# Kernel tuning notes

Measured on AMD Instinct MI355X. Metric: run time of the kernel, lower is better.

The kernel has to match this reference:

```python
import jax, jax.numpy as jnp
import numpy as np

EPS = 1e-5

def _ternary_ste(w):
    # STEQuantize: round(w/scale) clamped to [-1,1]; straight-through gradient.
    scale = jnp.maximum(jnp.mean(jnp.abs(w)), EPS)
    q = jnp.clip(jnp.round(w / scale), -1.0, 1.0)
    return w + jax.lax.stop_gradient(q - w)

def _bitlinear(x, w):
    # BitLinear: y = x @ (ternary(w) * scale)^T, scale = mean|w| (differentiable).
    scale = jnp.maximum(jnp.mean(jnp.abs(w)), EPS)
    return x @ (_ternary_ste(w) * scale).T

def _op_library(x, indices, weights, ops):
    # ops: (n_ops, D, D). Per-op ternary quantize + scale, then one batched einsum
    # instead of the python loop of small matmuls.
    n_ops = ops.shape[0]
    scales = jnp.maximum(jnp.mean(jnp.abs(ops), axis=(1, 2)), EPS)  # (n_ops,)
    q = jnp.clip(jnp.round(ops / scales[:, None, None]), -1.0, 1.0)
    w_eff = (ops + jax.lax.stop_gradient(q - ops)) * scales[:, None, None]  # (n,o,d)
    # transformed[n] = x @ w_eff[n]^T  ->  (B, S, n_ops, D)
    T = jnp.einsum('bsd,nod->bsno', x, w_eff)
    out = (1e-5 / n_ops) * jnp.sum(T, axis=2)
    gathered = jnp.take_along_axis(T, indices[:, :, :, None], axis=2)  # (B,S,K,D)
    out = out + jnp.sum(weights[..., None] * gathered, axis=2)
    return out

def _mem_read(x, slots, W_read):
    d = slots.shape[1]
    key = x @ W_read.T
    attn = jax.nn.softmax(key @ slots.T / jnp.sqrt(jnp.float32(d)), axis=-1)
    return attn @ slots

def _layernorm(x, gamma, beta):
    mu = jnp.mean(x, axis=-1, keepdims=True)
    var = jnp.var(x, axis=-1, keepdims=True)
    return (x - mu) * jax.lax.rsqrt(var + EPS) * gamma + beta

def _single_pass(reason, ops, W_router, slots, W_read, W_mix, ln_gamma, ln_beta, top_k):
    logits = _bitlinear(reason, W_router)              # (B,S,n_ops)
    vals, indices = jax.lax.top_k(logits, top_k)       # (B,S,K)
    weights = jax.nn.softmax(vals, axis=-1)
    op_out = _op_library(reason, indices, weights, ops)
    mem_out = _mem_read(reason, slots, W_read)
    mixed = jnp.concatenate([op_out, mem_out], axis=-1) @ W_mix.T
    return _layernorm(reason + mixed, ln_gamma, ln_beta)

def _write_signal(q, slots, W_wk, W_wg, W_wv):
    d = slots.shape[1]
    wk = q @ W_wk.T
    wg = jax.nn.sigmoid(q @ W_wg.T)                    # (B,S,1)
    wv = q @ W_wv.T
    addr = jax.nn.softmax(wk @ slots.T / jnp.sqrt(jnp.float32(d)), axis=-1)
    return wg * wv + 0.1 * (addr @ slots)

def setup_inputs() -> dict:
    key = jax.random.key(0)
    ks = jax.random.split(key, 12)
    B, S, d_model, d_reason = 8, 2048, 1024, 128
    n_ops, n_slots = 32, 16
    return {
        'hidden': jax.random.normal(ks[0], (B, S, d_model), jnp.float32),
        'force_depth': 2,
        'W_down': jax.random.normal(ks[1], (d_reason, d_model), jnp.float32) * 0.02,
        'W_up': jax.random.normal(ks[2], (d_model, d_reason), jnp.float32) * 0.02,
        'ops': jax.random.normal(ks[3], (n_ops, d_reason, d_reason), jnp.float32) * 0.02,
        'W_router': jax.random.normal(ks[4], (n_ops, d_reason), jnp.float32) * 0.02,
        'slots': jax.random.normal(ks[5], (n_slots, d_reason), jnp.float32) * 0.01,
        'W_read': jax.random.normal(ks[6], (d_reason, d_reason), jnp.float32) * 0.02,
        'W_wk': jax.random.normal(ks[7], (d_reason, d_reason), jnp.float32) * 0.02,
        'W_wg': jax.random.normal(ks[8], (1, d_reason), jnp.float32) * 0.02,
        'W_wv': jax.random.normal(ks[9], (d_reason, d_reason), jnp.float32) * 0.02,
        'W_mix': jax.random.normal(ks[10], (d_reason, 2 * d_reason), jnp.float32) * 0.02,
        'ln_gamma': jnp.ones((d_reason,), jnp.float32),
        'ln_beta': jnp.zeros((d_reason,), jnp.float32),
        'write_scale': jnp.float32(0.01),
    }

def reference(hidden, force_depth, W_down, W_up, ops, W_router, slots, W_read,
              W_wk, W_wg, W_wv, W_mix, ln_gamma, ln_beta, write_scale):
    top_k = 2
    reason = _bitlinear(hidden, W_down)
    for _ in range(int(force_depth)):
        reason = _single_pass(reason, ops, W_router, slots, W_read, W_mix,
                              ln_gamma, ln_beta, top_k)
    reason = reason + write_scale * _write_signal(reason, slots, W_wk, W_wg, W_wv)
    out = _bitlinear(reason, W_up)
    return hidden + out
```

## Files before the change

### kernel.cpp

```cpp
#include <hip/hip_runtime.h>


#define DR   128
#define DM   1024
#define NTOK 16384
#define NOPS 32
#define COEF (1e-5f / 32.f)

typedef __attribute__((ext_vector_type(8))) short bfrag;
typedef __attribute__((ext_vector_type(4))) float f32x4;

__device__ __forceinline__ ushort f2b_bits(float f) {
  union { float f; uint i; } c; c.f = f;
  uint x = c.i;
  return (ushort)((x + 0x7fffu + ((x >> 16) & 1u)) >> 16);
}
__device__ __forceinline__ float qeff(float w, float s) {
  float q = rintf(w / s);
  q = fminf(1.f, fmaxf(-1.f, q));
  return q * s;
}
__device__ __forceinline__ float waveRed(float v) {
#pragma unroll
  for (int m = 32; m > 0; m >>= 1) v += __shfl_xor(v, m, 64);
// ... 11 lines not shown
#define OFF_MRS     (OFF_WWVB + 32768)
#define OFF_MWS     (OFF_MRS + 8192)
#define OFF_SB      (OFF_MWS + 8192)
#define OFF_SLOTS   (OFF_SB + 8192)
#define OFF_WWG     (OFF_SLOTS + 8192)
#define OFF_GAMMA   (OFF_WWG + 512)
#define OFF_BETA    (OFF_GAMMA + 512)
#define OFF_WSC     (OFF_BETA + 512)
#define OFF_RF      (OFF_WSC + 256)
#define WS_TOTAL    (OFF_RF + 4194304)

__global__ __launch_bounds__(256) void k_absum_all(
    const float* __restrict__ W_down, const float* __restrict__ W_router,
    const float* __restrict__ W_up, const float* __restrict__ ops,
    float* __restrict__ sums) {
  __shared__ float ws4[4];
  const int y = blockIdx.y;
  const float* src; int n; float* dst;
  if (y == 0)      { src = W_down;   n = 131072; dst = &sums[0]; }
  else if (y == 1) { src = W_router; n = 4096;   dst = &sums[1]; }
  else if (y == 2) { src = W_up;     n = 131072; dst = &sums[2]; }
  else { src = ops + (size_t)(y - 3) * 16384; n = 16384; dst = &sums[y]; }
  float s = 0.f;
  for (int i = blockIdx.x * 256 + threadIdx.x; i < n; i += 8 * 256)
    s += fabsf(src[i]);
  s = waveRed(s);
  int lane = threadIdx.x & 63, wv = threadIdx.x >> 6;
  if (lane == 0) ws4[wv] = s;
  __syncthreads();
  if (threadIdx.x == 0) atomicAdd(dst, ws4[0] + ws4[1] + ws4[2] + ws4[3]);
}

__global__ __launch_bounds__(256) void k_build(
    const float* __restrict__ W_down, const float* __restrict__ W_up,
    const float* __restrict__ W_router, const float* __restrict__ ops,
    const float* __restrict__ W_read, const float* __restrict__ W_wk,
    const float* __restrict__ W_wg, const float* __restrict__ W_wv,
    const float* __restrict__ W_mix, const float* __restrict__ slots,
    const float* __restrict__ gamma, const float* __restrict__ beta,
    const float* __restrict__ wscale, int has_wsc, const float* __restrict__ sums,
    ushort* __restrict__ WdE, ushort* __restrict__ WuE, float* __restrict__ WrT,
    ushort* __restrict__ opsB, float* __restrict__ opsScale,
    ushort* __restrict__ WmixA, ushort* __restrict__ WwvB,
    float* __restrict__ Mrs, float* __restrict__ Mws, float* __restrict__ SBw,
    float* __restrict__ slotsF, float* __restrict__ WwgF,
    float* __restrict__ gammaF, float* __restrict__ betaF, float* __restrict__ wscF) {
  int id = blockIdx.x * 256 + threadIdx.x;
  const float s_wd = fmaxf(sums[0] * (1.f / 131072.f), 1e-5f);
  const float s_wr = fmaxf(sums[1] * (1.f / 4096.f), 1e-5f);
  const float s_wu = fmaxf(sums[2] * (1.f / 131072.f), 1e-5f);

  if (id < 131072) { WdE[id] = f2b_bits(qeff(W_down[id], s_wd)); return; }
  id -= 131072;
  if (id < 131072) { WuE[id] = f2b_bits(qeff(W_up[id], s_wu)); return; }
  id -= 131072;
  if (id < 4096) {
    int d = id >> 5, n = id & 31;
    WrT[id] = qeff(W_router[n * DR + d], s_wr);
    return;
  }
  id -= 4096;
  if (id < 524288) {
    int n = id >> 14;
    float s = fmaxf(sums[3 + n] * (1.f / 16384.f), 1e-5f);
    float q = rintf(ops[id] / s);
    q = fminf(1.f, fmaxf(-1.f, q));
    opsB[id] = f2b_bits(q);
    return;
  }
  id -= 524288;
  if (id < 32) { opsScale[id] = fmaxf(sums[3 + id] * (1.f / 16384.f), 1e-5f); return; }
  id -= 32;
  if (id < 16384) {
    int r = id >> 7, o = id & 127;
    WmixA[id] = f2b_bits(W_mix[r * 256 + o]);
    return;
  }
  id -= 16384;
  if (id < 16384) { WwvB[id] = f2b_bits(W_wv[id]); return; }
  id -= 16384;
  if (id < 2048) {
    int d = id >> 4, j = id & 15;
    float a = 0.f;
    for (int o = 0; o < DR; ++o) a += W_read[o * DR + d] * slots[j * DR + o];
    Mrs[id] = a;
    return;
  }
  id -= 2048;
  if (id < 2048) {
    int d = id >> 4, j = id & 15;
    float a = 0.f;
    for (int o = 0; o < DR; ++o) a += W_wk[o * DR + d] * slots[j * DR + o];
    Mws[id] = a;
    return;
  }
  id -= 2048;
  if (id < 2048) {
    int j = id >> 7, r = id & 127;
    float a = 0.f;
    for (int o = 0; o < DR; ++o) a += slots[j * DR + o] * W_mix[r * 256 + 128 + o];
    SBw[id] = a;
    return;
  }
  id -= 2048;
  if (id < 2048) { slotsF[id] = slots[id]; return; }
  id -= 2048;
  if (id < 128) { WwgF[id] = W_wg[id]; return; }
  id -= 128;
  if (id < 128) { gammaF[id] = gamma[id]; return; }
  id -= 128;
  if (id < 128) { betaF[id] = beta[id]; return; }
  id -= 128;
  if (id == 0) { wscF[0] = has_wsc ? wscale[0] : 0.01f; }
}

__global__ __launch_bounds__(256) void k_down(const float* __restrict__ hidden,
                                              const ushort* __restrict__ WdE,
                                              float* __restrict__ X) {
  const int w = threadIdx.x >> 6, lane = threadIdx.x & 63;
  const int quad = lane >> 4, mrow = lane & 15;
  const int m0 = blockIdx.x * 16;
  const int c0 = w * 32;

  f32x4 acc[2];
  acc[0] = (f32x4){0.f, 0.f, 0.f, 0.f};
  acc[1] = (f32x4){0.f, 0.f, 0.f, 0.f};

  const float* Ap = hidden + (size_t)(m0 + mrow) * DM + quad * 8;
#pragma unroll 2
  for (int kt = 0; kt < 32; ++kt) {
    float4 a0 = *(const float4*)(Ap + kt * 32);
    float4 a1 = *(const float4*)(Ap + kt * 32 + 4);
    bfrag a;
    a[0] = (short)f2b_bits(a0.x); a[1] = (short)f2b_bits(a0.y);
    a[2] = (short)f2b_bits(a0.z); a[3] = (short)f2b_bits(a0.w);
    a[4] = (short)f2b_bits(a1.x); a[5] = (short)f2b_bits(a1.y);
    a[6] = (short)f2b_bits(a1.z); a[7] = (short)f2b_bits(a1.w);
#pragma unroll
    for (int nt = 0; nt < 2; ++nt) {
      bfrag b = *(const bfrag*)(WdE + (size_t)(c0 + nt * 16 + mrow) * DM + kt * 32 + quad * 8);
      acc[nt] = __builtin_amdgcn_mfma_f32_16x16x32_bf16(a, b, acc[nt], 0, 0, 0);
    }
  }
#pragma unroll
  for (int nt = 0; nt < 2; ++nt)
#pragma unroll
    for (int r = 0; r < 4; ++r)
      X[(size_t)(m0 + quad * 4 + r) * DR + c0 + nt * 16 + mrow] = acc[nt][r];
}

__global__ __launch_bounds__(512) void k_pass2(
    float* __restrict__ X, ushort* __restrict__ RF, int emit,
    const float* __restrict__ WrT, const ushort* __restrict__ opsB,
    const float* __restrict__ opsScale, const ushort* __restrict__ WmixA,
    const float* __restrict__ Mrs, const float* __restrict__ SBw,
    const float* __restrict__ gammaF, const float* __restrict__ betaF,
    const ushort* __restrict__ WwvB, const float* __restrict__ Mws,
    const float* __restrict__ slotsF, const float* __restrict__ WwgF,
    const float* __restrict__ wscF) {
  __shared__ float  xsf[64][128];
  __shared__ ushort xsb[64][136];
  __shared__ float  lg[64][33];
  __shared__ float  coefT[32][64];
  __shared__ float  attn[64][17];
  __shared__ float  at2[64][17];
  __shared__ int    seli[64][2];
  __shared__ float  selw[64][2];
  __shared__ float  gp[64];
  __shared__ float  partS[8][4][4];
  __shared__ float  partQ[8][4][4];

  const int tid = threadIdx.x;
  const int w = tid >> 6, lane = tid & 63;
  const int quad = lane >> 4, mrow = lane & 15;
  const int t0 = blockIdx.x * 64;

  for (int i = tid; i < 2048; i += 512) {
    float4 v = *(const float4*)(X + (size_t)t0 * DR + i * 4);
    int t = i >> 5, c = (i & 31) * 4;
    xsf[t][c] = v.x; xsf[t][c + 1] = v.y; xsf[t][c + 2] = v.z; xsf[t][c + 3] = v.w;
    xsb[t][c] = f2b_bits(v.x); xsb[t][c + 1] = f2b_bits(v.y);
    xsb[t][c + 2] = f2b_bits(v.z); xsb[t][c + 3] = f2b_bits(v.w);
  }
  __syncthreads();

  for (int p = tid; p < 2048; p += 512) {
    int t = p >> 5, n = p & 31;
    float a = 0.f;
#pragma unroll 8
    for (int d = 0; d < DR; ++d) a += xsf[t][d] * WrT[d * 32 + n];
    lg[t][n] = a;
  }
  for (int p = tid; p < 1024; p += 512) {
    int t = p >> 4, j = p & 15;
    float a = 0.f;
#pragma unroll 8
    for (int d = 0; d < DR; ++d) a += xsf[t][d] * Mrs[d * 16 + j];
    attn[t][j] = a * 0.088388347648318447f;
  }
  __syncthreads();

  if (tid < 64) {
    float v0 = -1e30f; int i0 = 0;
#pragma unroll
    for (int n = 0; n < 32; ++n) { float v = lg[tid][n]; if (v > v0) { v0 = v; i0 = n; } }
    float v1 = -1e30f; int i1 = 0;
#pragma unroll
    for (int n = 0; n < 32; ++n)
      if (n != i0) { float v = lg[tid][n]; if (v > v1) { v1 = v; i1 = n; } }
    float e = expf(v1 - v0);
    float w0 = 1.f / (1.f + e);
    seli[tid][0] = i0; seli[tid][1] = i1;
    selw[tid][0] = w0; selw[tid][1] = e * w0;
    float m = -1e30f;
#pragma unroll
    for (int j = 0; j < 16; ++j) m = fmaxf(m, attn[tid][j]);
    float s = 0.f;
#pragma unroll
    for (int j = 0; j < 16; ++j) { float ee = expf(attn[tid][j] - m); attn[tid][j] = ee; s += ee; }
    float inv = 1.f / s;
#pragma unroll
    for (int j = 0; j < 16; ++j) attn[tid][j] *= inv;
  }
  __syncthreads();

  for (int p = tid; p < 2048; p += 512) {
    int n = p >> 6, t = p & 63;
    float cf = COEF;
    if (n == seli[t][0]) cf += selw[t][0];
    if (n == seli[t][1]) cf += selw[t][1];
    coefT[n][t] = cf * opsScale[n];
  }
  __syncthreads();

  bfrag a[4][4];
#pragma unroll
  for (int m = 0; m < 4; ++m)
#pragma unroll
    for (int kt = 0; kt < 4; ++kt)
      a[m][kt] = *(const bfrag*)&xsb[m * 16 + mrow][kt * 32 + quad * 8];

  const ushort* Bp = opsB + (size_t)(w * 16 + mrow) * DR + quad * 8;
  bfrag bc[4], bn[4];
#pragma unroll
  for (int kt = 0; kt < 4; ++kt) bc[kt] = *(const bfrag*)(Bp + kt * 32);

  f32x4 out[4];
#pragma unroll
  for (int m = 0; m < 4; ++m) out[m] = (f32x4){0.f, 0.f, 0.f, 0.f};

  for (int n = 0; n < NOPS; ++n) {
    if (n + 1 < NOPS) {
      const ushort* Bn = Bp + (size_t)(n + 1) * (DR * DR);
#pragma unroll
      for (int kt = 0; kt < 4; ++kt) bn[kt] = *(const bfrag*)(Bn + kt * 32);
    }
    f32x4 tmp[4];
#pragma unroll
    for (int m = 0; m < 4; ++m) tmp[m] = (f32x4){0.f, 0.f, 0.f, 0.f};
#pragma unroll
    for (int kt = 0; kt < 4; ++kt)
#pragma unroll
      for (int m = 0; m < 4; ++m)
        tmp[m] = __builtin_amdgcn_mfma_f32_16x16x32_bf16(a[m][kt], bc[kt], tmp[m], 0, 0, 0);
#pragma unroll
    for (int m = 0; m < 4; ++m) {
      f32x4 cf = *(const f32x4*)&coefT[n][m * 16 + quad * 4];
      out[m] += cf * tmp[m];
    }
    if (n + 1 < NOPS) {
#pragma unroll
      for (int kt = 0; kt < 4; ++kt) bc[kt] = bn[kt];
    }
  }
  __syncthreads();

#pragma unroll
  for (int m = 0; m < 4; ++m)
#pragma unroll
    for (int r = 0; r < 4; ++r)
      xsb[m * 16 + quad * 4 + r][w * 16 + mrow] = f2b_bits(out[m][r]);
  __syncthreads();

  const int mtile = w & 3;
  const int ch = (w >> 2) * 64;
  {
    bfrag a2[4];
#pragma unroll
    for (int kt = 0; kt < 4; ++kt)
      a2[kt] = *(const bfrag*)&xsb[mtile * 16 + mrow][kt * 32 + quad * 8];

    f32x4 acc[4];
#pragma unroll
    for (int i = 0; i < 4; ++i) acc[i] = (f32x4){0.f, 0.f, 0.f, 0.f};
#pragma unroll
    for (int kt = 0; kt < 4; ++kt)
#pragma unroll
      for (int nt = 0; nt < 4; ++nt) {
        bfrag b = *(const bfrag*)(WmixA + (size_t)(ch + nt * 16 + mrow) * DR + kt * 32 + quad * 8);
        acc[nt] = __builtin_amdgcn_mfma_f32_16x16x32_bf16(a2[kt], b, acc[nt], 0, 0, 0);
      }

    float v[4][4];
#pragma unroll
    for (int nt = 0; nt < 4; ++nt) {
      const int col = ch + nt * 16 + mrow;
#pragma unroll
      for (int r = 0; r < 4; ++r) {
        const int t = mtile * 16 + quad * 4 + r;
        float y0 = 0.f;
#pragma unroll
        for (int j = 0; j < 16; ++j) y0 += attn[t][j] * SBw[j * 128 + col];
        v[nt][r] = acc[nt][r] + xsf[t][col] + y0;
      }
    }
    float s[4], q[4];
#pragma unroll
    for (int r = 0; r < 4; ++r) {
      float ps = 0.f, pq = 0.f;
#pragma unroll
      for (int nt = 0; nt < 4; ++nt) { ps += v[nt][r]; pq += v[nt][r] * v[nt][r]; }
      s[r] = ps; q[r] = pq;
    }
#pragma unroll
    for (int m = 1; m < 16; m <<= 1)
#pragma unroll
      for (int r = 0; r < 4; ++r) {
        s[r] += __shfl_xor(s[r], m, 64);
        q[r] += __shfl_xor(q[r], m, 64);
      }
    if (mrow == 0)
#pragma unroll
      for (int r = 0; r < 4; ++r) { partS[w][quad][r] = s[r]; partQ[w][quad][r] = q[r]; }
    __syncthreads();

    float mu[4], rsd[4];
#pragma unroll
    for (int r = 0; r < 4; ++r) {
      float ts = s[r] + partS[w ^ 4][quad][r];
      float tq = q[r] + partQ[w ^ 4][quad][r];
      mu[r] = ts * (1.f / DR);
      float var = tq * (1.f / DR) - mu[r] * mu[r];
      rsd[r] = rsqrtf(var + 1e-5f);
    }
    if (!emit) {
#pragma unroll
      for (int nt = 0; nt < 4; ++nt) {
        const int col = ch + nt * 16 + mrow;
        const float g = gammaF[col], bb = betaF[col];
#pragma unroll
        for (int r = 0; r < 4; ++r) {
          const int t = mtile * 16 + quad * 4 + r;
          X[(size_t)(t0 + t) * DR + col] = (v[nt][r] - mu[r]) * rsd[r] * g + bb;
        }
      }
      return;
    }
#pragma unroll
    for (int nt = 0; nt < 4; ++nt) {
      const int col = ch + nt * 16 + mrow;
      const float g = gammaF[col], bb = betaF[col];
#pragma unroll
      for (int r = 0; r < 4; ++r) {
        const int t = mtile * 16 + quad * 4 + r;
        float val = (v[nt][r] - mu[r]) * rsd[r] * g + bb;
        xsf[t][col] = val;
        xsb[t][col] = f2b_bits(val);
      }
    }
  }
  __syncthreads();

  for (int p = tid; p < 1024; p += 512) {
    int t = p >> 4, j = p & 15;
    float a = 0.f;
#pragma unroll 8
    for (int d = 0; d < DR; ++d) a += xsf[t][d] * Mws[d * 16 + j];
    at2[t][j] = a * 0.088388347648318447f;
  }
  __syncthreads();

  if (tid < 64) {
    float z = 0.f;
#pragma unroll 8
    for (int d = 0; d < DR; ++d) z += xsf[tid][d] * WwgF[d];
    gp[tid] = wscF[0] / (1.f + expf(-z));
    float m = -1e30f;
#pragma unroll
    for (int j = 0; j < 16; ++j) m = fmaxf(m, at2[tid][j]);
    float s = 0.f;
#pragma unroll
    for (int j = 0; j < 16; ++j) { float e = expf(at2[tid][j] - m); at2[tid][j] = e; s += e; }
    float inv = 1.f / s;
#pragma unroll
    for (int j = 0; j < 16; ++j) at2[tid][j] *= inv;
  }
  __syncthreads();

  {
    bfrag a2[4];
#pragma unroll
    for (int kt = 0; kt < 4; ++kt)
      a2[kt] = *(const bfrag*)&xsb[mtile * 16 + mrow][kt * 32 + quad * 8];

    f32x4 acc[4];
#pragma unroll
    for (int i = 0; i < 4; ++i) acc[i] = (f32x4){0.f, 0.f, 0.f, 0.f};
#pragma unroll
    for (int kt = 0; kt < 4; ++kt)
#pragma unroll
      for (int nt = 0; nt < 4; ++nt) {
        bfrag b = *(const bfrag*)(WwvB + (size_t)(ch + nt * 16 + mrow) * DR + kt * 32 + quad * 8);
        acc[nt] = __builtin_amdgcn_mfma_f32_16x16x32_bf16(a2[kt], b, acc[nt], 0, 0, 0);
      }

    const float c01 = wscF[0] * 0.1f;
#pragma unroll
    for (int nt = 0; nt < 4; ++nt) {
      const int col = ch + nt * 16 + mrow;
#pragma unroll
      for (int r = 0; r < 4; ++r) {
        const int t = mtile * 16 + quad * 4 + r;
        float mo = 0.f;
#pragma unroll
        for (int j = 0; j < 16; ++j) mo += at2[t][j] * slotsF[j * DR + col];
        float val = xsf[t][col] + gp[t] * acc[nt][r] + c01 * mo;
        RF[(size_t)(t0 + t) * DR + col] = f2b_bits(val);
      }
    }
  }
}

__global__ __launch_bounds__(256) void k_up(const ushort* __restrict__ Rf,
                                            const ushort* __restrict__ WuE,
                                            const float* __restrict__ hidden,
                                            float* __restrict__ out) {
  __shared__ float cs[64][132];

  const int wave = threadIdx.x >> 6, lane = threadIdx.x & 63;
  const int quad = lane >> 4, mrow = lane & 15;
  const int mt = blockIdx.x >> 3, ngrp = blockIdx.x & 7;
  const int m0b = mt * 64;
  const int m0 = m0b + wave * 16;
  const int c0 = ngrp * 128;

  f32x4 acc[8];
#pragma unroll
  for (int i = 0; i < 8; ++i) acc[i] = (f32x4){0.f, 0.f, 0.f, 0.f};

  const ushort* Ap = Rf + (size_t)(m0 + mrow) * DR + quad * 8;
#pragma unroll
  for (int kt = 0; kt < 4; ++kt) {
    bfrag a = *(const bfrag*)(Ap + kt * 32);
#pragma unroll
    for (int nt = 0; nt < 8; ++nt) {
      const ushort* Bp = WuE + (size_t)(c0 + nt * 16 + mrow) * DR + kt * 32 + quad * 8;
      bfrag b = *(const bfrag*)Bp;
      acc[nt] = __builtin_amdgcn_mfma_f32_16x16x32_bf16(a, b, acc[nt], 0, 0, 0);
    }
  }
#pragma unroll
  for (int nt = 0; nt < 8; ++nt)
#pragma unroll
    for (int r = 0; r < 4; ++r)
      cs[wave * 16 + quad * 4 + r][nt * 16 + mrow] = acc[nt][r];
  __syncthreads();

#pragma unroll
  for (int k = 0; k < 8; ++k) {
    const int i = threadIdx.x + k * 256;
    const int t = i >> 5, c4 = (i & 31) * 4;
    const size_t idx = (size_t)(m0b + t) * DM + c0 + c4;
    float4 h = *(const float4*)(hidden + idx);
    float4 v;
    v.x = h.x + cs[t][c4];
    v.y = h.y + cs[t][c4 + 1];
    v.z = h.z + cs[t][c4 + 2];
    v.w = h.w + cs[t][c4 + 3];
    *(float4*)(out + idx) = v;
  }
}

extern "C" void kernel_launch(void* const* d_in, const int* in_sizes, int n_in,
                              void* d_out, int out_size, void* d_ws, size_t ws_size,
                              hipStream_t stream) {
  int ns[20]; int nn = 0; int lastsc = -1;
  for (int i = 0; i < n_in; ++i) {
    if (in_sizes[i] == 1) lastsc = i;
    else if (nn < 20) ns[nn++] = i;
  }
  int iH = 0, iWd = 2, iWu = 3, iOps = 4, iWr = 5, iSl = 6, iRe = 7,
      iWk = 8, iWg = 9, iWv = 10, iMx = 11, iG = 12, iB = 13;
  if (nn >= 13) {
    iH  = ns[0];  iWd = ns[1];  iWu = ns[2];  iOps = ns[3]; iWr = ns[4];
    iSl = ns[5];  iRe = ns[6];  iWk = ns[7];  iWg = ns[8];  iWv = ns[9];
    iMx = ns[10]; iG  = ns[11]; iB  = ns[12];
  }
  const float* hidden   = (const float*)d_in[iH];
  const float* W_down   = (const float*)d_in[iWd];
  const float* W_up     = (const float*)d_in[iWu];
  const float* opsw     = (const float*)d_in[iOps];
  const float* W_router = (const float*)d_in[iWr];
  const float* slots    = (const float*)d_in[iSl];
  const float* W_read   = (const float*)d_in[iRe];
  const float* W_wk     = (const float*)d_in[iWk];
  const float* W_wg     = (const float*)d_in[iWg];
  const float* W_wv     = (const float*)d_in[iWv];
  const float* W_mix    = (const float*)d_in[iMx];
  const float* lng      = (const float*)d_in[iG];
  const float* lnb      = (const float*)d_in[iB];
  const float* wscale   = (lastsc >= 0) ? (const float*)d_in[lastsc] : (const float*)d_in[iG];
  const int has_wsc     = (lastsc >= 0) ? 1 : 0;

  char* ws = (char*)d_ws;
  float*  sums   = (float*)(ws + OFF_SUMS);
  float*  opsSc  = (float*)(ws + OFF_OPSSC);
  ushort* WdE    = (ushort*)(ws + OFF_WDE);
  ushort* WuE    = (ushort*)(ws + OFF_WUE);
  float*  WrT    = (float*)(ws + OFF_WRT);
  ushort* opsB   = (ushort*)(ws + OFF_OPSB);
  ushort* WmixA  = (ushort*)(ws + OFF_WMIXA);
  ushort* WwvB   = (ushort*)(ws + OFF_WWVB);
  float*  Mrs    = (float*)(ws + OFF_MRS);
  float*  Mws    = (float*)(ws + OFF_MWS);
  float*  SBw    = (float*)(ws + OFF_SB);
  float*  slotsF = (float*)(ws + OFF_SLOTS);
  float*  WwgF   = (float*)(ws + OFF_WWG);
  float*  gammaF = (float*)(ws + OFF_GAMMA);
  float*  betaF  = (float*)(ws + OFF_BETA);
  float*  wscF   = (float*)(ws + OFF_WSC);
  ushort* RF     = (ushort*)(ws + OFF_RF);

  float* X = (float*)d_out;

  hipMemsetAsync(ws + OFF_SUMS, 0, 256, stream);
  k_absum_all<<<dim3(8, 35), 256, 0, stream>>>(W_down, W_router, W_up, opsw, sums);
  k_build<<<3250, 256, 0, stream>>>(W_down, W_up, W_router, opsw, W_read, W_wk, W_wg,
                                    W_wv, W_mix, slots, lng, lnb, wscale, has_wsc,
                                    sums, WdE, WuE, WrT, opsB, opsSc, WmixA, WwvB,
                                    Mrs, Mws, SBw, slotsF, WwgF, gammaF, betaF, wscF);
  k_down<<<1024, 256, 0, stream>>>(hidden, WdE, X);
  k_pass2<<<256, 512, 0, stream>>>(X, RF, 0, WrT, opsB, opsSc, WmixA, Mrs, SBw,
                                   gammaF, betaF, WwvB, Mws, slotsF, WwgF, wscF);
  k_pass2<<<256, 512, 0, stream>>>(X, RF, 1, WrT, opsB, opsSc, WmixA, Mrs, SBw,
                                   gammaF, betaF, WwvB, Mws, slotsF, WwgF, wscF);
  k_up<<<2048, 256, 0, stream>>>(RF, WuE, hidden, X);
}
```

Baseline: 386.3 us.

## Halve k_pass2 token tile to 32 rows and double grid to 512 blocks

```diff
diff --git a/kernel.cpp b/kernel.cpp
--- a/kernel.cpp
+++ b/kernel.cpp
@@ -184,7 +184,7 @@
       X[(size_t)(m0 + quad * 4 + r) * DR + c0 + nt * 16 + mrow] = acc[nt][r];
 }
 
-__global__ __launch_bounds__(512) void k_pass2(
+__global__ __launch_bounds__(512, 4) void k_pass2(
     float* __restrict__ X, ushort* __restrict__ RF, int emit,
     const float* __restrict__ WrT, const ushort* __restrict__ opsB,
     const float* __restrict__ opsScale, const ushort* __restrict__ WmixA,
@@ -193,24 +193,24 @@
     const ushort* __restrict__ WwvB, const float* __restrict__ Mws,
     const float* __restrict__ slotsF, const float* __restrict__ WwgF,
     const float* __restrict__ wscF) {
-  __shared__ float  xsf[64][128];
-  __shared__ ushort xsb[64][136];
-  __shared__ float  lg[64][33];
-  __shared__ float  coefT[32][64];
-  __shared__ float  attn[64][17];
-  __shared__ float  at2[64][17];
-  __shared__ int    seli[64][2];
-  __shared__ float  selw[64][2];
-  __shared__ float  gp[64];
+  __shared__ float  xsf[32][128];
+  __shared__ ushort xsb[32][136];
+  __shared__ float  lg[32][33];
+  __shared__ float  coefT[32][32];
+  __shared__ float  attn[32][17];
+  __shared__ float  at2[32][17];
+  __shared__ int    seli[32][2];
+  __shared__ float  selw[32][2];
+  __shared__ float  gp[32];
   __shared__ float  partS[8][4][4];
   __shared__ float  partQ[8][4][4];
 
   const int tid = threadIdx.x;
   const int w = tid >> 6, lane = tid & 63;
   const int quad = lane >> 4, mrow = lane & 15;
-  const int t0 = blockIdx.x * 64;
-
-  for (int i = tid; i < 2048; i += 512) {
+  const int t0 = blockIdx.x * 32;
+
+  for (int i = tid; i < 1024; i += 512) {
     float4 v = *(const float4*)(X + (size_t)t0 * DR + i * 4);
     int t = i >> 5, c = (i & 31) * 4;
     xsf[t][c] = v.x; xsf[t][c + 1] = v.y; xsf[t][c + 2] = v.z; xsf[t][c + 3] = v.w;
@@ -219,23 +219,37 @@
   }
   __syncthreads();
 
-  for (int p = tid; p < 2048; p += 512) {
+  for (int p = tid; p < 1024; p += 512) {
     int t = p >> 5, n = p & 31;
+    const float4* xr = (const float4*)&xsf[t][0];
     float a = 0.f;
 #pragma unroll 8
-    for (int d = 0; d < DR; ++d) a += xsf[t][d] * WrT[d * 32 + n];
+    for (int d4 = 0; d4 < 32; ++d4) {
+      float4 x = xr[d4];
+      a += x.x * WrT[(d4 * 4 + 0) * 32 + n];
+      a += x.y * WrT[(d4 * 4 + 1) * 32 + n];
+      a += x.z * WrT[(d4 * 4 + 2) * 32 + n];
+      a += x.w * WrT[(d4 * 4 + 3) * 32 + n];
+    }
     lg[t][n] = a;
   }
-  for (int p = tid; p < 1024; p += 512) {
-    int t = p >> 4, j = p & 15;
+  {
+    int t = tid >> 4, j = tid & 15;
+    const float4* xr = (const float4*)&xsf[t][0];
     float a = 0.f;
 #pragma unroll 8
-    for (int d = 0; d < DR; ++d) a += xsf[t][d] * Mrs[d * 16 + j];
+    for (int d4 = 0; d4 < 32; ++d4) {
+      float4 x = xr[d4];
+      a += x.x * Mrs[(d4 * 4 + 0) * 16 + j];
+      a += x.y * Mrs[(d4 * 4 + 1) * 16 + j];
+      a += x.z * Mrs[(d4 * 4 + 2) * 16 + j];
+      a += x.w * Mrs[(d4 * 4 + 3) * 16 + j];
+    }
     attn[t][j] = a * 0.088388347648318447f;
   }
   __syncthreads();
 
-  if (tid < 64) {
+  if (tid < 32) {
     float v0 = -1e30f; int i0 = 0;
 #pragma unroll
     for (int n = 0; n < 32; ++n) { float v = lg[tid][n]; if (v > v0) { v0 = v; i0 = n; } }
@@ -247,20 +261,22 @@
     float w0 = 1.f / (1.f + e);
     seli[tid][0] = i0; seli[tid][1] = i1;
     selw[tid][0] = w0; selw[tid][1] = e * w0;
+  } else if (tid >= 64 && tid < 96) {
+    const int t = tid - 64;
     float m = -1e30f;
 #pragma unroll
-    for (int j = 0; j < 16; ++j) m = fmaxf(m, attn[tid][j]);
+    for (int j = 0; j < 16; ++j) m = fmaxf(m, attn[t][j]);
     float s = 0.f;
 #pragma unroll
-    for (int j = 0; j < 16; ++j) { float ee = expf(attn[tid][j] - m); attn[tid][j] = ee; s += ee; }
+    for (int j = 0; j < 16; ++j) { float ee = expf(attn[t][j] - m); attn[t][j] = ee; s += ee; }
     float inv = 1.f / s;
 #pragma unroll
-    for (int j = 0; j < 16; ++j) attn[tid][j] *= inv;
-  }
-  __syncthreads();
-
-  for (int p = tid; p < 2048; p += 512) {
-    int n = p >> 6, t = p & 63;
+    for (int j = 0; j < 16; ++j) attn[t][j] *= inv;
+  }
+  __syncthreads();
+
+  for (int p = tid; p < 1024; p += 512) {
+    int n = p >> 5, t = p & 31;
     float cf = COEF;
     if (n == seli[t][0]) cf += selw[t][0];
     if (n == seli[t][1]) cf += selw[t][1];
@@ -268,9 +284,9 @@
   }
   __syncthreads();
 
-  bfrag a[4][4];
-#pragma unroll
-  for (int m = 0; m < 4; ++m)
+  bfrag a[2][4];
+#pragma unroll
+  for (int m = 0; m < 2; ++m)
 #pragma unroll
     for (int kt = 0; kt < 4; ++kt)
       a[m][kt] = *(const bfrag*)&xsb[m * 16 + mrow][kt * 32 + quad * 8];
@@ -280,9 +296,9 @@
 #pragma unroll
   for (int kt = 0; kt < 4; ++kt) bc[kt] = *(const bfrag*)(Bp + kt * 32);
 
-  f32x4 out[4];
-#pragma unroll
-  for (int m = 0; m < 4; ++m) out[m] = (f32x4){0.f, 0.f, 0.f, 0.f};
+  f32x4 out[2];
+#pragma unroll
+  for (int m = 0; m < 2; ++m) out[m] = (f32x4){0.f, 0.f, 0.f, 0.f};
 
   for (int n = 0; n < NOPS; ++n) {
     if (n + 1 < NOPS) {
@@ -290,16 +306,16 @@
 #pragma unroll
       for (int kt = 0; kt < 4; ++kt) bn[kt] = *(const bfrag*)(Bn + kt * 32);
     }
-    f32x4 tmp[4];
-#pragma unroll
-    for (int m = 0; m < 4; ++m) tmp[m] = (f32x4){0.f, 0.f, 0.f, 0.f};
+    f32x4 tmp[2];
+#pragma unroll
+    for (int m = 0; m < 2; ++m) tmp[m] = (f32x4){0.f, 0.f, 0.f, 0.f};
 #pragma unroll
     for (int kt = 0; kt < 4; ++kt)
 #pragma unroll
-      for (int m = 0; m < 4; ++m)
+      for (int m = 0; m < 2; ++m)
         tmp[m] = __builtin_amdgcn_mfma_f32_16x16x32_bf16(a[m][kt], bc[kt], tmp[m], 0, 0, 0);
 #pragma unroll
-    for (int m = 0; m < 4; ++m) {
+    for (int m = 0; m < 2; ++m) {
       f32x4 cf = *(const f32x4*)&coefT[n][m * 16 + quad * 4];
       out[m] += cf * tmp[m];
     }
@@ -311,34 +327,34 @@
   __syncthreads();
 
 #pragma unroll
-  for (int m = 0; m < 4; ++m)
+  for (int m = 0; m < 2; ++m)
 #pragma unroll
     for (int r = 0; r < 4; ++r)
       xsb[m * 16 + quad * 4 + r][w * 16 + mrow] = f2b_bits(out[m][r]);
   __syncthreads();
 
-  const int mtile = w & 3;
-  const int ch = (w >> 2) * 64;
+  const int mtile = w & 1;
+  const int ch = (w >> 1) * 32;
   {
     bfrag a2[4];
 #pragma unroll
     for (int kt = 0; kt < 4; ++kt)
       a2[kt] = *(const bfrag*)&xsb[mtile * 16 + mrow][kt * 32 + quad * 8];
 
-    f32x4 acc[4];
-#pragma unroll
-    for (int i = 0; i < 4; ++i) acc[i] = (f32x4){0.f, 0.f, 0.f, 0.f};
+    f32x4 acc[2];
+#pragma unroll
+    for (int i = 0; i < 2; ++i) acc[i] = (f32x4){0.f, 0.f, 0.f, 0.f};
 #pragma unroll
     for (int kt = 0; kt < 4; ++kt)
 #pragma unroll
-      for (int nt = 0; nt < 4; ++nt) {
+      for (int nt = 0; nt < 2; ++nt) {
         bfrag b = *(const bfrag*)(WmixA + (size_t)(ch + nt * 16 + mrow) * DR + kt * 32 + quad * 8);
         acc[nt] = __builtin_amdgcn_mfma_f32_16x16x32_bf16(a2[kt], b, acc[nt], 0, 0, 0);
       }
 
-    float v[4][4];
-#pragma unroll
-    for (int nt = 0; nt < 4; ++nt) {
+    float v[2][4];
+#pragma unroll
+    for (int nt = 0; nt < 2; ++nt) {
       const int col = ch + nt * 16 + mrow;
 #pragma unroll
       for (int r = 0; r < 4; ++r) {
@@ -354,7 +370,7 @@
     for (int r = 0; r < 4; ++r) {
       float ps = 0.f, pq = 0.f;
 #pragma unroll
-      for (int nt = 0; nt < 4; ++nt) { ps += v[nt][r]; pq += v[nt][r] * v[nt][r]; }
+      for (int nt = 0; nt < 2; ++nt) { ps += v[nt][r]; pq += v[nt][r] * v[nt][r]; }
       s[r] = ps; q[r] = pq;
     }
 #pragma unroll
@@ -372,15 +388,15 @@
     float mu[4], rsd[4];
 #pragma unroll
     for (int r = 0; r < 4; ++r) {
-      float ts = s[r] + partS[w ^ 4][quad][r];
-      float tq = q[r] + partQ[w ^ 4][quad][r];
+      float ts = s[r] + partS[w ^ 2][quad][r] + partS[w ^ 4][quad][r] + partS[w ^ 6][quad][r];
+      float tq = q[r] + partQ[w ^ 2][quad][r] + partQ[w ^ 4][quad][r] + partQ[w ^ 6][quad][r];
       mu[r] = ts * (1.f / DR);
       float var = tq * (1.f / DR) - mu[r] * mu[r];
       rsd[r] = rsqrtf(var + 1e-5f);
     }
     if (!emit) {
 #pragma unroll
-      for (int nt = 0; nt < 4; ++nt) {
+      for (int nt = 0; nt < 2; ++nt) {
         const int col = ch + nt * 16 + mrow;
         const float g = gammaF[col], bb = betaF[col];
 #pragma unroll
@@ -392,7 +408,7 @@
       return;
     }
 #pragma unroll
-    for (int nt = 0; nt < 4; ++nt) {
+    for (int nt = 0; nt < 2; ++nt) {
       const int col = ch + nt * 16 + mrow;
       const float g = gammaF[col], bb = betaF[col];
 #pragma unroll
@@ -406,29 +422,43 @@
   }
   __syncthreads();
 
-  for (int p = tid; p < 1024; p += 512) {
-    int t = p >> 4, j = p & 15;
+  {
+    int t = tid >> 4, j = tid & 15;
+    const float4* xr = (const float4*)&xsf[t][0];
     float a = 0.f;
 #pragma unroll 8
-    for (int d = 0; d < DR; ++d) a += xsf[t][d] * Mws[d * 16 + j];
+    for (int d4 = 0; d4 < 32; ++d4) {
+      float4 x = xr[d4];
+      a += x.x * Mws[(d4 * 4 + 0) * 16 + j];
+      a += x.y * Mws[(d4 * 4 + 1) * 16 + j];
+      a += x.z * Mws[(d4 * 4 + 2) * 16 + j];
+      a += x.w * Mws[(d4 * 4 + 3) * 16 + j];
+    }
     at2[t][j] = a * 0.088388347648318447f;
   }
   __syncthreads();
 
-  if (tid < 64) {
+  if (tid < 32) {
+    const float4* xr = (const float4*)&xsf[tid][0];
     float z = 0.f;
 #pragma unroll 8
-    for (int d = 0; d < DR; ++d) z += xsf[tid][d] * WwgF[d];
+    for (int d4 = 0; d4 < 32; ++d4) {
+      float4 x = xr[d4];
+      z += x.x * WwgF[d4 * 4 + 0] + x.y * WwgF[d4 * 4 + 1]
+         + x.z * WwgF[d4 * 4 + 2] + x.w * WwgF[d4 * 4 + 3];
+    }
     gp[tid] = wscF[0] / (1.f + expf(-z));
+  } else if (tid >= 64 && tid < 96) {
+    const int t = tid - 64;
     float m = -1e30f;
 #pragma unroll
-    for (int j = 0; j < 16; ++j) m = fmaxf(m, at2[tid][j]);
+    for (int j = 0; j < 16; ++j) m = fmaxf(m, at2[t][j]);
     float s = 0.f;
 #pragma unroll
-    for (int j = 0; j < 16; ++j) { float e = expf(at2[tid][j] - m); at2[tid][j] = e; s += e; }
+    for (int j = 0; j < 16; ++j) { float e = expf(at2[t][j] - m); at2[t][j] = e; s += e; }
     float inv = 1.f / s;
 #pragma unroll
-    for (int j = 0; j < 16; ++j) at2[tid][j] *= inv;
+    for (int j = 0; j < 16; ++j) at2[t][j] *= inv;
   }
   __syncthreads();
 
@@ -438,20 +468,20 @@
     for (int kt = 0; kt < 4; ++kt)
       a2[kt] = *(const bfrag*)&xsb[mtile * 16 + mrow][kt * 32 + quad * 8];
 
-    f32x4 acc[4];
-#pragma unroll
-    for (int i = 0; i < 4; ++i) acc[i] = (f32x4){0.f, 0.f, 0.f, 0.f};
+    f32x4 acc[2];
+#pragma unroll
+    for (int i = 0; i < 2; ++i) acc[i] = (f32x4){0.f, 0.f, 0.f, 0.f};
 #pragma unroll
     for (int kt = 0; kt < 4; ++kt)
 #pragma unroll
-      for (int nt = 0; nt < 4; ++nt) {
+      for (int nt = 0; nt < 2; ++nt) {
         bfrag b = *(const bfrag*)(WwvB + (size_t)(ch + nt * 16 + mrow) * DR + kt * 32 + quad * 8);
         acc[nt] = __builtin_amdgcn_mfma_f32_16x16x32_bf16(a2[kt], b, acc[nt], 0, 0, 0);
       }
 
     const float c01 = wscF[0] * 0.1f;
 #pragma unroll
-    for (int nt = 0; nt < 4; ++nt) {
+    for (int nt = 0; nt < 2; ++nt) {
       const int col = ch + nt * 16 + mrow;
 #pragma unroll
       for (int r = 0; r < 4; ++r) {
@@ -575,9 +605,9 @@
                                     sums, WdE, WuE, WrT, opsB, opsSc, WmixA, WwvB,
                                     Mrs, Mws, SBw, slotsF, WwgF, gammaF, betaF, wscF);
   k_down<<<1024, 256, 0, stream>>>(hidden, WdE, X);
-  k_pass2<<<256, 512, 0, stream>>>(X, RF, 0, WrT, opsB, opsSc, WmixA, Mrs, SBw,
+  k_pass2<<<512, 512, 0, stream>>>(X, RF, 0, WrT, opsB, opsSc, WmixA, Mrs, SBw,
                                    gammaF, betaF, WwvB, Mws, slotsF, WwgF, wscF);
-  k_pass2<<<256, 512, 0, stream>>>(X, RF, 1, WrT, opsB, opsSc, WmixA, Mrs, SBw,
+  k_pass2<<<512, 512, 0, stream>>>(X, RF, 1, WrT, opsB, opsSc, WmixA, Mrs, SBw,
                                    gammaF, betaF, WwvB, Mws, slotsF, WwgF, wscF);
   k_up<<<2048, 256, 0, stream>>>(RF, WuE, hidden, X);
 }
```

After: 437.6 us. 13.3% more time.

## Fuse down-projection and both reasoning passes into one persistent-tile kernel

Applied to the files above, without the earlier changes.

```diff
diff --git a/kernel.cpp b/kernel.cpp
--- a/kernel.cpp
+++ b/kernel.cpp
@@ -117,6 +117,7 @@
   if (id < 2048) {
     int d = id >> 4, j = id & 15;
     float a = 0.f;
+#pragma unroll 8
     for (int o = 0; o < DR; ++o) a += W_read[o * DR + d] * slots[j * DR + o];
     Mrs[id] = a;
     return;
@@ -125,6 +126,7 @@
   if (id < 2048) {
     int d = id >> 4, j = id & 15;
     float a = 0.f;
+#pragma unroll 8
     for (int o = 0; o < DR; ++o) a += W_wk[o * DR + d] * slots[j * DR + o];
     Mws[id] = a;
     return;
@@ -133,6 +135,7 @@
   if (id < 2048) {
     int j = id >> 7, r = id & 127;
     float a = 0.f;
+#pragma unroll 8
     for (int o = 0; o < DR; ++o) a += slots[j * DR + o] * W_mix[r * 256 + 128 + o];
     SBw[id] = a;
     return;
@@ -149,43 +152,9 @@
   if (id == 0) { wscF[0] = has_wsc ? wscale[0] : 0.01f; }
 }
 
-__global__ __launch_bounds__(256) void k_down(const float* __restrict__ hidden,
-                                              const ushort* __restrict__ WdE,
-                                              float* __restrict__ X) {
-  const int w = threadIdx.x >> 6, lane = threadIdx.x & 63;
-  const int quad = lane >> 4, mrow = lane & 15;
-  const int m0 = blockIdx.x * 16;
-  const int c0 = w * 32;
-
-  f32x4 acc[2];
-  acc[0] = (f32x4){0.f, 0.f, 0.f, 0.f};
-  acc[1] = (f32x4){0.f, 0.f, 0.f, 0.f};
-
-  const float* Ap = hidden + (size_t)(m0 + mrow) * DM + quad * 8;
-#pragma unroll 2
-  for (int kt = 0; kt < 32; ++kt) {
-    float4 a0 = *(const float4*)(Ap + kt * 32);
-    float4 a1 = *(const float4*)(Ap + kt * 32 + 4);
-    bfrag a;
-    a[0] = (short)f2b_bits(a0.x); a[1] = (short)f2b_bits(a0.y);
-    a[2] = (short)f2b_bits(a0.z); a[3] = (short)f2b_bits(a0.w);
-    a[4] = (short)f2b_bits(a1.x); a[5] = (short)f2b_bits(a1.y);
-    a[6] = (short)f2b_bits(a1.z); a[7] = (short)f2b_bits(a1.w);
-#pragma unroll
-    for (int nt = 0; nt < 2; ++nt) {
-      bfrag b = *(const bfrag*)(WdE + (size_t)(c0 + nt * 16 + mrow) * DM + kt * 32 + quad * 8);
-      acc[nt] = __builtin_amdgcn_mfma_f32_16x16x32_bf16(a, b, acc[nt], 0, 0, 0);
-    }
-  }
-#pragma unroll
-  for (int nt = 0; nt < 2; ++nt)
-#pragma unroll
-    for (int r = 0; r < 4; ++r)
-      X[(size_t)(m0 + quad * 4 + r) * DR + c0 + nt * 16 + mrow] = acc[nt][r];
-}
-
-__global__ __launch_bounds__(512) void k_pass2(
-    float* __restrict__ X, ushort* __restrict__ RF, int emit,
+__global__ __launch_bounds__(512) void k_fused(
+    const float* __restrict__ hidden, const ushort* __restrict__ WdE,
+    ushort* __restrict__ RF,
     const float* __restrict__ WrT, const ushort* __restrict__ opsB,
     const float* __restrict__ opsScale, const ushort* __restrict__ WmixA,
     const float* __restrict__ Mrs, const float* __restrict__ SBw,
@@ -193,7 +162,7 @@
     const ushort* __restrict__ WwvB, const float* __restrict__ Mws,
     const float* __restrict__ slotsF, const float* __restrict__ WwgF,
     const float* __restrict__ wscF) {
-  __shared__ float  xsf[64][128];
+  __shared__ float  xsf[64][132];
   __shared__ ushort xsb[64][136];
   __shared__ float  lg[64][33];
   __shared__ float  coefT[32][64];
@@ -210,175 +179,225 @@
   const int quad = lane >> 4, mrow = lane & 15;
   const int t0 = blockIdx.x * 64;
 
-  for (int i = tid; i < 2048; i += 512) {
-    float4 v = *(const float4*)(X + (size_t)t0 * DR + i * 4);
-    int t = i >> 5, c = (i & 31) * 4;
-    xsf[t][c] = v.x; xsf[t][c + 1] = v.y; xsf[t][c + 2] = v.z; xsf[t][c + 3] = v.w;
-    xsb[t][c] = f2b_bits(v.x); xsb[t][c + 1] = f2b_bits(v.y);
-    xsb[t][c + 2] = f2b_bits(v.z); xsb[t][c + 3] = f2b_bits(v.w);
+  {
+    f32x4 dacc[4];
+#pragma unroll
+    for (int m = 0; m < 4; ++m) dacc[m] = (f32x4){0.f, 0.f, 0.f, 0.f};
+
+    for (int kc = 0; kc < 8; ++kc) {
+      for (int i = tid; i < 2048; i += 512) {
+        int t = i >> 5, c = (i & 31) * 4;
+        float4 v = *(const float4*)(hidden + (size_t)(t0 + t) * DM + kc * 128 + c);
+        xsb[t][c] = f2b_bits(v.x); xsb[t][c + 1] = f2b_bits(v.y);
+        xsb[t][c + 2] = f2b_bits(v.z); xsb[t][c + 3] = f2b_bits(v.w);
+      }
+      __syncthreads();
+#pragma unroll
+      for (int kt = 0; kt < 4; ++kt) {
+        bfrag b = *(const bfrag*)(WdE + (size_t)(w * 16 + mrow) * DM + kc * 128 + kt * 32 + quad * 8);
+#pragma unroll
+        for (int m = 0; m < 4; ++m) {
+          bfrag a = *(const bfrag*)&xsb[m * 16 + mrow][kt * 32 + quad * 8];
+          dacc[m] = __builtin_amdgcn_mfma_f32_16x16x32_bf16(a, b, dacc[m], 0, 0, 0);
+        }
+      }
+      __syncthreads();
+    }
+#pragma unroll
+    for (int m = 0; m < 4; ++m)
+#pragma unroll
+      for (int r = 0; r < 4; ++r) {
+        float v = dacc[m][r];
+        xsf[m * 16 + quad * 4 + r][w * 16 + mrow] = v;
+        xsb[m * 16 + quad * 4 + r][w * 16 + mrow] = f2b_bits(v);
+      }
   }
   __syncthreads();
 
-  for (int p = tid; p < 2048; p += 512) {
-    int t = p >> 5, n = p & 31;
-    float a = 0.f;
+  for (int pass = 0; pass < 2; ++pass) {
+    for (int p = tid; p < 2048; p += 512) {
+      int t = p >> 5, n = p & 31;
+      const float4* xr = (const float4*)&xsf[t][0];
+      float a = 0.f;
 #pragma unroll 8
-    for (int d = 0; d < DR; ++d) a += xsf[t][d] * WrT[d * 32 + n];
-    lg[t][n] = a;
-  }
-  for (int p = tid; p < 1024; p += 512) {
-    int t = p >> 4, j = p & 15;
-    float a = 0.f;
+      for (int d4 = 0; d4 < 32; ++d4) {
+        float4 x = xr[d4];
+        a += x.x * WrT[(d4 * 4 + 0) * 32 + n];
+        a += x.y * WrT[(d4 * 4 + 1) * 32 + n];
+        a += x.z * WrT[(d4 * 4 + 2) * 32 + n];
+        a += x.w * WrT[(d4 * 4 + 3) * 32 + n];
+      }
+      lg[t][n] = a;
+    }
+    for (int p = tid; p < 1024; p += 512) {
+      int t = p >> 4, j = p & 15;
+      const float4* xr = (const float4*)&xsf[t][0];
+      float a = 0.f;
 #pragma unroll 8
-    for (int d = 0; d < DR; ++d) a += xsf[t][d] * Mrs[d * 16 + j];
-    attn[t][j] = a * 0.088388347648318447f;
-  }
-  __syncthreads();
-
-  if (tid < 64) {
-    float v0 = -1e30f; int i0 = 0;
-#pragma unroll
-    for (int n = 0; n < 32; ++n) { float v = lg[tid][n]; if (v > v0) { v0 = v; i0 = n; } }
-    float v1 = -1e30f; int i1 = 0;
-#pragma unroll
-    for (int n = 0; n < 32; ++n)
-      if (n != i0) { float v = lg[tid][n]; if (v > v1) { v1 = v; i1 = n; } }
-    float e = expf(v1 - v0);
-    float w0 = 1.f / (1.f + e);
-    seli[tid][0] = i0; seli[tid][1] = i1;
-    selw[tid][0] = w0; selw[tid][1] = e * w0;
-    float m = -1e30f;
-#pragma unroll
-    for (int j = 0; j < 16; ++j) m = fmaxf(m, attn[tid][j]);
-    float s = 0.f;
-#pragma unroll
-    for (int j = 0; j < 16; ++j) { float ee = expf(attn[tid][j] - m); attn[tid][j] = ee; s += ee; }
-    float inv = 1.f / s;
-#pragma unroll
-    for (int j = 0; j < 16; ++j) attn[tid][j] *= inv;
-  }
-  __syncthreads();
-
-  for (int p = tid; p < 2048; p += 512) {
-    int n = p >> 6, t = p & 63;
-    float cf = COEF;
-    if (n == seli[t][0]) cf += selw[t][0];
-    if (n == seli[t][1]) cf += selw[t][1];
-    coefT[n][t] = cf * opsScale[n];
-  }
-  __syncthreads();
-
-  bfrag a[4][4];
-#pragma unroll
-  for (int m = 0; m < 4; ++m)
-#pragma unroll
-    for (int kt = 0; kt < 4; ++kt)
-      a[m][kt] = *(const bfrag*)&xsb[m * 16 + mrow][kt * 32 + quad * 8];
-
-  const ushort* Bp = opsB + (size_t)(w * 16 + mrow) * DR + quad * 8;
-  bfrag bc[4], bn[4];
-#pragma unroll
-  for (int kt = 0; kt < 4; ++kt) bc[kt] = *(const bfrag*)(Bp + kt * 32);
-
-  f32x4 out[4];
-#pragma unroll
-  for (int m = 0; m < 4; ++m) out[m] = (f32x4){0.f, 0.f, 0.f, 0.f};
-
-  for (int n = 0; n < NOPS; ++n) {
-    if (n + 1 < NOPS) {
-      const ushort* Bn = Bp + (size_t)(n + 1) * (DR * DR);
-#pragma unroll
-      for (int kt = 0; kt < 4; ++kt) bn[kt] = *(const bfrag*)(Bn + kt * 32);
-    }
-    f32x4 tmp[4];
-#pragma unroll
-    for (int m = 0; m < 4; ++m) tmp[m] = (f32x4){0.f, 0.f, 0.f, 0.f};
-#pragma unroll
-    for (int kt = 0; kt < 4; ++kt)
+      for (int d4 = 0; d4 < 32; ++d4) {
+        float4 x = xr[d4];
+        a += x.x * Mrs[(d4 * 4 + 0) * 16 + j];
+        a += x.y * Mrs[(d4 * 4 + 1) * 16 + j];
+        a += x.z * Mrs[(d4 * 4 + 2) * 16 + j];
+        a += x.w * Mrs[(d4 * 4 + 3) * 16 + j];
+      }
+      attn[t][j] = a * 0.088388347648318447f;
+    }
+    __syncthreads();
+
+    if (tid < 64) {
+      float v0 = -1e30f; int i0 = 0;
+#pragma unroll
+      for (int n = 0; n < 32; ++n) { float v = lg[tid][n]; if (v > v0) { v0 = v; i0 = n; } }
+      float v1 = -1e30f; int i1 = 0;
+#pragma unroll
+      for (int n = 0; n < 32; ++n)
+        if (n != i0) { float v = lg[tid][n]; if (v > v1) { v1 = v; i1 = n; } }
+      float e = expf(v1 - v0);
+      float w0 = 1.f / (1.f + e);
+      seli[tid][0] = i0; seli[tid][1] = i1;
+      selw[tid][0] = w0; selw[tid][1] = e * w0;
+    } else if (tid < 128) {
+      const int t = tid - 64;
+      float m = -1e30f;
+#pragma unroll
+      for (int j = 0; j < 16; ++j) m = fmaxf(m, attn[t][j]);
+      float s = 0.f;
+#pragma unroll
+      for (int j = 0; j < 16; ++j) { float ee = expf(attn[t][j] - m); attn[t][j] = ee; s += ee; }
+      float inv = 1.f / s;
+#pragma unroll
+      for (int j = 0; j < 16; ++j) attn[t][j] *= inv;
+    }
+    __syncthreads();
+
+    for (int p = tid; p < 2048; p += 512) {
+      int n = p >> 6, t = p & 63;
+      float cf = COEF;
+      if (n == seli[t][0]) cf += selw[t][0];
+      if (n == seli[t][1]) cf += selw[t][1];
+      coefT[n][t] = cf * opsScale[n];
+    }
+    __syncthreads();
+
+    f32x4 out[4];
+    {
+      bfrag a[4][4];
 #pragma unroll
       for (int m = 0; m < 4; ++m)
-        tmp[m] = __builtin_amdgcn_mfma_f32_16x16x32_bf16(a[m][kt], bc[kt], tmp[m], 0, 0, 0);
-#pragma unroll
-    for (int m = 0; m < 4; ++m) {
-      f32x4 cf = *(const f32x4*)&coefT[n][m * 16 + quad * 4];
-      out[m] += cf * tmp[m];
-    }
-    if (n + 1 < NOPS) {
-#pragma unroll
-      for (int kt = 0; kt < 4; ++kt) bc[kt] = bn[kt];
-    }
-  }
-  __syncthreads();
-
-#pragma unroll
-  for (int m = 0; m < 4; ++m)
-#pragma unroll
-    for (int r = 0; r < 4; ++r)
-      xsb[m * 16 + quad * 4 + r][w * 16 + mrow] = f2b_bits(out[m][r]);
-  __syncthreads();
-
-  const int mtile = w & 3;
-  const int ch = (w >> 2) * 64;
-  {
-    bfrag a2[4];
-#pragma unroll
-    for (int kt = 0; kt < 4; ++kt)
-      a2[kt] = *(const bfrag*)&xsb[mtile * 16 + mrow][kt * 32 + quad * 8];
-
-    f32x4 acc[4];
-#pragma unroll
-    for (int i = 0; i < 4; ++i) acc[i] = (f32x4){0.f, 0.f, 0.f, 0.f};
-#pragma unroll
-    for (int kt = 0; kt < 4; ++kt)
+#pragma unroll
+        for (int kt = 0; kt < 4; ++kt)
+          a[m][kt] = *(const bfrag*)&xsb[m * 16 + mrow][kt * 32 + quad * 8];
+
+      const ushort* Bp = opsB + (size_t)(w * 16 + mrow) * DR + quad * 8;
+      bfrag bc[4], bn[4];
+#pragma unroll
+      for (int kt = 0; kt < 4; ++kt) bc[kt] = *(const bfrag*)(Bp + kt * 32);
+
+      f32x4 cfc[4], cfn[4];
+#pragma unroll
+      for (int m = 0; m < 4; ++m) {
+        out[m] = (f32x4){0.f, 0.f, 0.f, 0.f};
+        cfc[m] = *(const f32x4*)&coefT[0][m * 16 + quad * 4];
+      }
+
+      for (int n = 0; n < NOPS; ++n) {
+        if (n + 1 < NOPS) {
+          const ushort* Bn = Bp + (size_t)(n + 1) * (DR * DR);
+#pragma unroll
+          for (int kt = 0; kt < 4; ++kt) bn[kt] = *(const bfrag*)(Bn + kt * 32);
+#pragma unroll
+          for (int m = 0; m < 4; ++m)
+            cfn[m] = *(const f32x4*)&coefT[n + 1][m * 16 + quad * 4];
+        }
+        f32x4 tmp[4];
+#pragma unroll
+        for (int m = 0; m < 4; ++m) tmp[m] = (f32x4){0.f, 0.f, 0.f, 0.f};
+#pragma unroll
+        for (int kt = 0; kt < 4; ++kt)
+#pragma unroll
+          for (int m = 0; m < 4; ++m)
+            tmp[m] = __builtin_amdgcn_mfma_f32_16x16x32_bf16(a[m][kt], bc[kt], tmp[m], 0, 0, 0);
+#pragma unroll
+        for (int m = 0; m < 4; ++m) out[m] += cfc[m] * tmp[m];
+        if (n + 1 < NOPS) {
+#pragma unroll
+          for (int kt = 0; kt < 4; ++kt) bc[kt] = bn[kt];
+#pragma unroll
+          for (int m = 0; m < 4; ++m) cfc[m] = cfn[m];
+        }
+      }
+    }
+    __syncthreads();
+
+#pragma unroll
+    for (int m = 0; m < 4; ++m)
+#pragma unroll
+      for (int r = 0; r < 4; ++r)
+        xsb[m * 16 + quad * 4 + r][w * 16 + mrow] = f2b_bits(out[m][r]);
+    __syncthreads();
+
+    const int mtile = w & 3;
+    const int ch = (w >> 2) * 64;
+    {
+      bfrag a2[4];
+#pragma unroll
+      for (int kt = 0; kt < 4; ++kt)
+        a2[kt] = *(const bfrag*)&xsb[mtile * 16 + mrow][kt * 32 + quad * 8];
+
+      f32x4 acc[4];
+#pragma unroll
+      for (int i = 0; i < 4; ++i) acc[i] = (f32x4){0.f, 0.f, 0.f, 0.f};
+#pragma unroll
+      for (int kt = 0; kt < 4; ++kt)
+#pragma unroll
+        for (int nt = 0; nt < 4; ++nt) {
+          bfrag b = *(const bfrag*)(WmixA + (size_t)(ch + nt * 16 + mrow) * DR + kt * 32 + quad * 8);
+          acc[nt] = __builtin_amdgcn_mfma_f32_16x16x32_bf16(a2[kt], b, acc[nt], 0, 0, 0);
+        }
+
+      float v[4][4];
 #pragma unroll
       for (int nt = 0; nt < 4; ++nt) {
-        bfrag b = *(const bfrag*)(WmixA + (size_t)(ch + nt * 16 + mrow) * DR + kt * 32 + quad * 8);
-        acc[nt] = __builtin_amdgcn_mfma_f32_16x16x32_bf16(a2[kt], b, acc[nt], 0, 0, 0);
-      }
-
-    float v[4][4];
-#pragma unroll
-    for (int nt = 0; nt < 4; ++nt) {
-      const int col = ch + nt * 16 + mrow;
+        const int col = ch + nt * 16 + mrow;
+#pragma unroll
+        for (int r = 0; r < 4; ++r) {
+          const int t = mtile * 16 + quad * 4 + r;
+          float y0 = 0.f;
+#pragma unroll
+          for (int j = 0; j < 16; ++j) y0 += attn[t][j] * SBw[j * 128 + col];
+          v[nt][r] = acc[nt][r] + xsf[t][col] + y0;
+        }
+      }
+      float s[4], q[4];
 #pragma unroll
       for (int r = 0; r < 4; ++r) {
-        const int t = mtile * 16 + quad * 4 + r;
-        float y0 = 0.f;
-#pragma unroll
-        for (int j = 0; j < 16; ++j) y0 += attn[t][j] * SBw[j * 128 + col];
-        v[nt][r] = acc[nt][r] + xsf[t][col] + y0;
-      }
-    }
-    float s[4], q[4];
-#pragma unroll
-    for (int r = 0; r < 4; ++r) {
-      float ps = 0.f, pq = 0.f;
-#pragma unroll
-      for (int nt = 0; nt < 4; ++nt) { ps += v[nt][r]; pq += v[nt][r] * v[nt][r]; }
-      s[r] = ps; q[r] = pq;
-    }
-#pragma unroll
-    for (int m = 1; m < 16; m <<= 1)
+        float ps = 0.f, pq = 0.f;
+#pragma unroll
+        for (int nt = 0; nt < 4; ++nt) { ps += v[nt][r]; pq += v[nt][r] * v[nt][r]; }
+        s[r] = ps; q[r] = pq;
+      }
+#pragma unroll
+      for (int m = 1; m < 16; m <<= 1)
+#pragma unroll
+        for (int r = 0; r < 4; ++r) {
+          s[r] += __shfl_xor(s[r], m, 64);
+          q[r] += __shfl_xor(q[r], m, 64);
+        }
+      if (mrow == 0)
+#pragma unroll
+        for (int r = 0; r < 4; ++r) { partS[w][quad][r] = s[r]; partQ[w][quad][r] = q[r]; }
+      __syncthreads();
+
+      float mu[4], rsd[4];
 #pragma unroll
       for (int r = 0; r < 4; ++r) {
-        s[r] += __shfl_xor(s[r], m, 64);
-        q[r] += __shfl_xor(q[r], m, 64);
-      }
-    if (mrow == 0)
-#pragma unroll
-      for (int r = 0; r < 4; ++r) { partS[w][quad][r] = s[r]; partQ[w][quad][r] = q[r]; }
-    __syncthreads();
-
-    float mu[4], rsd[4];
-#pragma unroll
-    for (int r = 0; r < 4; ++r) {
-      float ts = s[r] + partS[w ^ 4][quad][r];
-      float tq = q[r] + partQ[w ^ 4][quad][r];
-      mu[r] = ts * (1.f / DR);
-      float var = tq * (1.f / DR) - mu[r] * mu[r];
-      rsd[r] = rsqrtf(var + 1e-5f);
-    }
-    if (!emit) {
+        float ts = s[r] + partS[w ^ 4][quad][r];
+        float tq = q[r] + partQ[w ^ 4][quad][r];
+        mu[r] = ts * (1.f / DR);
+        float var = tq * (1.f / DR) - mu[r] * mu[r];
+        rsd[r] = rsqrtf(var + 1e-5f);
+      }
 #pragma unroll
       for (int nt = 0; nt < 4; ++nt) {
         const int col = ch + nt * 16 + mrow;
@@ -386,53 +405,58 @@
 #pragma unroll
         for (int r = 0; r < 4; ++r) {
           const int t = mtile * 16 + quad * 4 + r;
-          X[(size_t)(t0 + t) * DR + col] = (v[nt][r] - mu[r]) * rsd[r] * g + bb;
+          float val = (v[nt][r] - mu[r]) * rsd[r] * g + bb;
+          xsf[t][col] = val;
+          xsb[t][col] = f2b_bits(val);
         }
       }
-      return;
-    }
-#pragma unroll
-    for (int nt = 0; nt < 4; ++nt) {
-      const int col = ch + nt * 16 + mrow;
-      const float g = gammaF[col], bb = betaF[col];
-#pragma unroll
-      for (int r = 0; r < 4; ++r) {
-        const int t = mtile * 16 + quad * 4 + r;
-        float val = (v[nt][r] - mu[r]) * rsd[r] * g + bb;
-        xsf[t][col] = val;
-        xsb[t][col] = f2b_bits(val);
-      }
-    }
-  }
-  __syncthreads();
+    }
+    __syncthreads();
+  }
 
   for (int p = tid; p < 1024; p += 512) {
     int t = p >> 4, j = p & 15;
+    const float4* xr = (const float4*)&xsf[t][0];
     float a = 0.f;
 #pragma unroll 8
-    for (int d = 0; d < DR; ++d) a += xsf[t][d] * Mws[d * 16 + j];
+    for (int d4 = 0; d4 < 32; ++d4) {
+      float4 x = xr[d4];
+      a += x.x * Mws[(d4 * 4 + 0) * 16 + j];
+      a += x.y * Mws[(d4 * 4 + 1) * 16 + j];
+      a += x.z * Mws[(d4 * 4 + 2) * 16 + j];
+      a += x.w * Mws[(d4 * 4 + 3) * 16 + j];
+    }
     at2[t][j] = a * 0.088388347648318447f;
   }
   __syncthreads();
 
   if (tid < 64) {
+    const float4* xr = (const float4*)&xsf[tid][0];
     float z = 0.f;
 #pragma unroll 8
-    for (int d = 0; d < DR; ++d) z += xsf[tid][d] * WwgF[d];
+    for (int d4 = 0; d4 < 32; ++d4) {
+      float4 x = xr[d4];
+      z += x.x * WwgF[d4 * 4 + 0] + x.y * WwgF[d4 * 4 + 1]
+         + x.z * WwgF[d4 * 4 + 2] + x.w * WwgF[d4 * 4 + 3];
+    }
     gp[tid] = wscF[0] / (1.f + expf(-z));
+  } else if (tid < 128) {
+    const int t = tid - 64;
     float m = -1e30f;
 #pragma unroll
-    for (int j = 0; j < 16; ++j) m = fmaxf(m, at2[tid][j]);
+    for (int j = 0; j < 16; ++j) m = fmaxf(m, at2[t][j]);
     float s = 0.f;
 #pragma unroll
-    for (int j = 0; j < 16; ++j) { float e = expf(at2[tid][j] - m); at2[tid][j] = e; s += e; }
+    for (int j = 0; j < 16; ++j) { float e = expf(at2[t][j] - m); at2[t][j] = e; s += e; }
     float inv = 1.f / s;
 #pragma unroll
-    for (int j = 0; j < 16; ++j) at2[tid][j] *= inv;
+    for (int j = 0; j < 16; ++j) at2[t][j] *= inv;
   }
   __syncthreads();
 
   {
+    const int mtile = w & 3;
+    const int ch = (w >> 2) * 64;
     bfrag a2[4];
 #pragma unroll
     for (int kt = 0; kt < 4; ++kt)
@@ -574,10 +598,7 @@
                                     W_wv, W_mix, slots, lng, lnb, wscale, has_wsc,
                                     sums, WdE, WuE, WrT, opsB, opsSc, WmixA, WwvB,
                                     Mrs, Mws, SBw, slotsF, WwgF, gammaF, betaF, wscF);
-  k_down<<<1024, 256, 0, stream>>>(hidden, WdE, X);
-  k_pass2<<<256, 512, 0, stream>>>(X, RF, 0, WrT, opsB, opsSc, WmixA, Mrs, SBw,
-                                   gammaF, betaF, WwvB, Mws, slotsF, WwgF, wscF);
-  k_pass2<<<256, 512, 0, stream>>>(X, RF, 1, WrT, opsB, opsSc, WmixA, Mrs, SBw,
-                                   gammaF, betaF, WwvB, Mws, slotsF, WwgF, wscF);
+  k_fused<<<256, 512, 0, stream>>>(hidden, WdE, RF, WrT, opsB, opsSc, WmixA, Mrs,
+                                   SBw, gammaF, betaF, WwvB, Mws, slotsF, WwgF, wscF);
   k_up<<<2048, 256, 0, stream>>>(RF, WuE, hidden, X);
 }
```

Result: slower. 656.0 us (+69.8%).
